# Kernel optimization log

Hardware: AMD Instinct MI355X
Metric: run time of the kernel (lower is better)

Reference implementation:

```python
import jax, jax.numpy as jnp
import numpy as np

B, N, E, H = 2, 2048, 2048, 16
D = E // H  # head_dim = 128


def setup_inputs() -> dict:
    key = jax.random.key(0)
    k1, k2, k3, k4 = jax.random.split(key, 4)
    x = jax.random.normal(k1, (B, N, E), dtype=jnp.float32)
    Wq = jax.random.normal(k2, (E, E), dtype=jnp.float32) * 0.02
    Wkv = jax.random.normal(k3, (2 * E, E), dtype=jnp.float32) * 0.02
    Wout = jax.random.normal(k4, (E, E), dtype=jnp.float32) * 0.02
    return {"x": x, "Wq": Wq, "Wkv": Wkv, "Wout": Wout}


def reference(x, Wq, Wkv, Wout):
    # projections (torch Linear: y = x @ W.T)
    q = x @ Wq.T                      # [b, n, e]
    kv = x @ Wkv.T                    # [b, n, 2e]
    k, v = jnp.split(kv, 2, axis=-1)  # each [b, n, e]

    def split_heads(t):
        return t.reshape(B, N, H, D).transpose(0, 2, 1, 3)  # [b, h, n, d]

    q, k, v = split_heads(q), split_heads(k), split_heads(v)

    scale = D ** -0.5
    sim = jnp.einsum('bhid,bhjd->bhij', q * scale, k)  # [b, h, n, n]

    # causal mask: triu(j - i + 1) masks strictly-future positions
    mask_value = -jnp.finfo(sim.dtype).max
    causal_mask = jnp.triu(jnp.ones((N, N), dtype=bool), k=1)
    sim = jnp.where(causal_mask, mask_value, sim)

    attn = jax.nn.softmax(sim, axis=-1)
    out = jnp.einsum('bhij,bhjd->bhid', attn, v)  # [b, h, n, d]
    out = out.transpose(0, 2, 1, 3).reshape(B, N, E)
    return out @ Wout.T
```

## Files before the change

kernel.cpp:

```cpp
#include <hip/hip_runtime.h>


typedef __bf16 bf16;
typedef bf16 bf16x4 __attribute__((ext_vector_type(4)));
typedef bf16 bf16x8 __attribute__((ext_vector_type(8)));
typedef float f32x4 __attribute__((ext_vector_type(4)));
typedef float f32x16 __attribute__((ext_vector_type(16)));

typedef const __attribute__((address_space(1))) void cg_void;
typedef __attribute__((address_space(3))) void lds_void;

#define MFMA16(a, b, c) __builtin_amdgcn_mfma_f32_16x16x32_bf16((a), (b), (c), 0, 0, 0)
#define MFMA32(a, b, c) __builtin_amdgcn_mfma_f32_32x32x16_bf16((a), (b), (c), 0, 0, 0)

__device__ __forceinline__ void async_load16(const bf16* g, bf16* l) {
  __builtin_amdgcn_global_load_lds((cg_void*)g, (lds_void*)l, 16, 0, 0);
}

__global__ __launch_bounds__(256) void cast_all_kernel(
    const float* __restrict__ x, const float* __restrict__ wq,
    const float* __restrict__ wkv, const float* __restrict__ wout,
    bf16* __restrict__ xb, bf16* __restrict__ wqkvb, bf16* __restrict__ woutb) {
  long i = (long)blockIdx.x * 256 + threadIdx.x;
  const float* src; bf16* dst; long off;
  if (i < 1048576)      { src = x;    dst = xb;            off = i; }
  else if (i < 2621440) { src = wq;   dst = wqkvb;         off = i - 1048576;
                          if (off >= 524288) { src = wkv; dst = wqkvb + 4194304; off -= 524288; } }
  else                  { src = wout; dst = woutb;         off = i - 2621440; }
  float4 f0 = ((const float4*)src)[2 * off];
  float4 f1 = ((const float4*)src)[2 * off + 1];
  bf16x8 o;
  o[0] = (bf16)f0.x; o[1] = (bf16)f0.y; o[2] = (bf16)f0.z; o[3] = (bf16)f0.w;
  o[4] = (bf16)f1.x; o[5] = (bf16)f1.y; o[6] = (bf16)f1.z; o[7] = (bf16)f1.w;
  ((bf16x8*)dst)[off] = o;
}

template <typename OutT>
__global__ __launch_bounds__(256, 2)
void gemm_bt_kernel(const bf16* __restrict__ A, const bf16* __restrict__ B,
                    OutT* __restrict__ C, int K, int NN) {
  __shared__ __attribute__((aligned(16))) bf16 As[128 * 32];
  __shared__ __attribute__((aligned(16))) bf16 Bs[128 * 32];
  const int tid = threadIdx.x;
  const int wave = tid >> 6, lane = tid & 63;
  const int quad = lane >> 4, l15 = lane & 15;
  const int m0 = blockIdx.y * 128, n0 = blockIdx.x * 128;
  const int wm = (wave >> 1) * 64, wn = (wave & 1) * 64;

  f32x4 acc[4][4];
#pragma unroll
  for (int i = 0; i < 4; ++i)
#pragma unroll
    for (int j = 0; j < 4; ++j) acc[i][j] = {0.f, 0.f, 0.f, 0.f};

  const int srow = tid >> 2;
  const int scol = (tid & 3) * 8;
  const bf16* aG = A + (size_t)(m0 + srow) * K + scol;
  const bf16* bG = B + (size_t)(n0 + srow) * K + scol;
  bf16* aL = As + srow * 32 + scol;
  bf16* bL = Bs + srow * 32 + scol;
  const size_t gstep = (size_t)64 * K;

  for (int kt = 0; kt < K; kt += 32) {
    __syncthreads();
    async_load16(aG, aL);
    async_load16(aG + gstep, aL + 64 * 32);
    async_load16(bG, bL);
    async_load16(bG + gstep, bL + 64 * 32);
    aG += 32; bG += 32;
    __syncthreads();

    bf16x8 af[4], bfr[4];
#pragma unroll
    for (int i = 0; i < 4; ++i)
      af[i] = *(const bf16x8*)(As + (wm + i * 16 + l15) * 32 + quad * 8);
#pragma unroll
    for (int j = 0; j < 4; ++j)
      bfr[j] = *(const bf16x8*)(Bs + (wn + j * 16 + l15) * 32 + quad * 8);
#pragma unroll
    for (int i = 0; i < 4; ++i)
#pragma unroll
      for (int j = 0; j < 4; ++j) acc[i][j] = MFMA16(af[i], bfr[j], acc[i][j]);
  }

#pragma unroll
  for (int i = 0; i < 4; ++i) {
#pragma unroll
    for (int r = 0; r < 4; ++r) {
      int row = m0 + wm + i * 16 + quad * 4 + r;
      size_t base = (size_t)row * NN + n0 + wn + l15;
#pragma unroll
      for (int j = 0; j < 4; ++j) C[base + j * 16] = (OutT)acc[i][j][r];
    }
  }
}

__global__ __launch_bounds__(256) void vtrans_kernel(const bf16* __restrict__ qkvb,
                                                     bf16* __restrict__ vt) {
  constexpr int QKV = 6144, NSEQ = 2048, E = 2048;
  __shared__ __attribute__((aligned(16))) bf16 Ts[64 * 64];
  const int t = threadIdx.x;
  const int n0 = blockIdx.x * 64, f0 = blockIdx.y * 64, bb = blockIdx.z;
#pragma unroll
  for (int p = 0; p < 2; ++p) {
    int c = p * 256 + t;
    int i = c >> 3, jc = c & 7;
    bf16x8 v = *(const bf16x8*)(qkvb + (size_t)(bb * NSEQ + n0 + i) * QKV + 4096 + f0 + jc * 8);
    *(bf16x8*)(Ts + i * 64 + ((jc + i) & 7) * 8) = v;
  }
  __syncthreads();
#pragma unroll
  for (int p = 0; p < 2; ++p) {
    int c = p * 256 + t;
    int fl = c >> 3, nl = (c & 7) * 8;
    bf16x8 o;
#pragma unroll
    for (int k = 0; k < 8; ++k) {
      int row = nl + k;
      o[k] = Ts[row * 64 + (((fl >> 3) + row) & 7) * 8 + (fl & 7)];
    }
    *(bf16x8*)(vt + (size_t)(bb * E + f0 + fl) * NSEQ + n0 + nl) = o;
  }
}

__global__ __launch_bounds__(128, 2)
void attn_kernel(const bf16* __restrict__ qkv, const bf16* __restrict__ vt,
                 bf16* __restrict__ yb) {
  constexpr int NSEQ = 2048, E = 2048, QKV = 6144;
  __shared__ __attribute__((aligned(16))) bf16 Ks[64 * 128];
  __shared__ __attribute__((aligned(16))) bf16 Vs[128 * 64];
  __shared__ __attribute__((aligned(16))) bf16 Ps[2][32 * 64];
  const int tid = threadIdx.x;
  const int wave = tid >> 6, lane = tid & 63;
  const int l31 = lane & 31, half = lane >> 5;
  const int b = blockIdx.x >> 4, h = blockIdx.x & 15;
  const int slot = blockIdx.y, qsub = slot & 7, g = slot >> 3;
  const int qt = (g == 0) ? qsub : (g == 1) ? 15 - qsub : (g == 2) ? 16 + qsub : 31 - qsub;
  const float c1 = 0.08838834764831845f * 1.44269504088896f;

  const int qrow = qt * 64 + wave * 32 + l31;
  bf16x8 qf[8];
  {
    const bf16* qp = qkv + (size_t)(b * NSEQ + qrow) * QKV + h * 128 + half * 8;
#pragma unroll
    for (int k8 = 0; k8 < 8; ++k8) qf[k8] = *(const bf16x8*)(qp + k8 * 16);
  }

  float m = -3.0e38f, l = 0.f;
  f32x16 accO[4];
#pragma unroll
  for (int md = 0; md < 4; ++md)
#pragma unroll
    for (int r = 0; r < 16; ++r) accO[md][r] = 0.f;

  bf16* psw = Ps[wave];
  const int ksr = tid >> 4, kss = tid & 15;
  const int vsr = tid >> 3, vss = tid & 7;
  bf16* kdst = Ks + tid * 8;
  bf16* vdst = Vs + tid * 8;

  for (int kt = 0; kt <= qt; ++kt) {
    __syncthreads();
#pragma unroll
    for (int p = 0; p < 8; ++p) {
      int r = p * 8 + ksr;
      int gch = kss ^ (r & 7);
      const bf16* gsrc = qkv + (size_t)(b * NSEQ + kt * 64 + r) * QKV + 2048 + h * 128 + gch * 8;
      async_load16(gsrc, kdst + p * 1024);
    }
#pragma unroll
    for (int p = 0; p < 8; ++p) {
      int r = p * 16 + vsr;
      int gch = vss ^ (r & 7);
      const bf16* gsrc = vt + ((size_t)b * E + h * 128 + r) * NSEQ + kt * 64 + gch * 8;
      async_load16(gsrc, vdst + p * 1024);
    }
    __syncthreads();

    f32x16 st[2];
#pragma unroll
    for (int mt = 0; mt < 2; ++mt)
#pragma unroll
      for (int r = 0; r < 16; ++r) st[mt][r] = 0.f;
#pragma unroll
    for (int k8 = 0; k8 < 8; ++k8) {
#pragma unroll
      for (int mt = 0; mt < 2; ++mt) {
        int row = mt * 32 + l31;
        int sl = (k8 * 2 + half) ^ (row & 7);
        bf16x8 kf = *(const bf16x8*)(Ks + row * 128 + sl * 8);
        st[mt] = MFMA32(kf, qf[k8], st[mt]);
      }
    }

    if (kt == qt) {
#pragma unroll
      for (int mt = 0; mt < 2; ++mt)
#pragma unroll
        for (int r = 0; r < 16; ++r) {
          int t = kt * 64 + mt * 32 + (r & 3) + 8 * (r >> 2) + 4 * half;
          if (t > qrow) st[mt][r] = -3.0e38f;
        }
    }

    float mx = -3.0e38f;
#pragma unroll
    for (int mt = 0; mt < 2; ++mt)
#pragma unroll
      for (int r = 0; r < 16; ++r) mx = fmaxf(mx, st[mt][r]);
    mx = fmaxf(mx, __shfl_xor(mx, 32));
    float mnew = fmaxf(m, mx);
    float alpha = exp2f((m - mnew) * c1);
    float mc = mnew * c1;
    m = mnew;
    float psum = 0.f;
#pragma unroll
    for (int mt = 0; mt < 2; ++mt)
#pragma unroll
      for (int r = 0; r < 16; ++r) {
        float p = exp2f(st[mt][r] * c1 - mc);
        psum += p;
        int t = mt * 32 + (r & 3) + 8 * (r >> 2) + 4 * half;
        psw[l31 * 64 + ((t >> 3) ^ (l31 & 7)) * 8 + (t & 7)] = (bf16)p;
      }
    psum += __shfl_xor(psum, 32);
    l = l * alpha + psum;

    if (alpha != 1.0f) {
#pragma unroll
      for (int md = 0; md < 4; ++md)
#pragma unroll
        for (int r = 0; r < 16; ++r) accO[md][r] *= alpha;
    }

    bf16x8 pf[4];
#pragma unroll
    for (int kk = 0; kk < 4; ++kk) {
      int sl = (kk * 2 + half) ^ (l31 & 7);
      pf[kk] = *(const bf16x8*)(psw + l31 * 64 + sl * 8);
    }
#pragma unroll
    for (int md = 0; md < 4; ++md) {
      int row = md * 32 + l31;
#pragma unroll
      for (int kk = 0; kk < 4; ++kk) {
        int sl = (kk * 2 + half) ^ (row & 7);
        bf16x8 vf = *(const bf16x8*)(Vs + row * 64 + sl * 8);
        accO[md] = MFMA32(vf, pf[kk], accO[md]);
      }
    }
  }

  float invl = 1.0f / l;
  bf16* yp = yb + (size_t)(b * NSEQ + qrow) * E + h * 128;
#pragma unroll
  for (int md = 0; md < 4; ++md)
#pragma unroll
    for (int rq = 0; rq < 4; ++rq) {
      bf16x4 o;
#pragma unroll
      for (int i = 0; i < 4; ++i) o[i] = (bf16)(accO[md][rq * 4 + i] * invl);
      *(bf16x4*)(yp + md * 32 + rq * 8 + half * 4) = o;
    }
}

extern "C" void kernel_launch(void* const* d_in, const int* in_sizes, int n_in,
                              void* d_out, int out_size, void* d_ws, size_t ws_size,
                              hipStream_t stream) {
  const float* x    = (const float*)d_in[0];
  const float* Wq   = (const float*)d_in[1];
  const float* Wkv  = (const float*)d_in[2];
  const float* Wout = (const float*)d_in[3];
  float* out = (float*)d_out;

  constexpr size_t NX = (size_t)2 * 2048 * 2048;
  constexpr size_t NW = (size_t)2048 * 2048;

  bf16* xb     = (bf16*)d_ws;
  bf16* wqkvb  = xb + NX;
  bf16* woutb  = wqkvb + 3 * NW;
  bf16* qkv_b  = woutb + NW;
  bf16* y_b    = qkv_b + 3 * NX;
  bf16* vt_b   = xb;

  cast_all_kernel<<<12288, 256, 0, stream>>>(x, Wq, Wkv, Wout, xb, wqkvb, woutb);

  gemm_bt_kernel<bf16><<<dim3(48, 32), 256, 0, stream>>>(xb, wqkvb, qkv_b, 2048, 6144);
  vtrans_kernel<<<dim3(32, 32, 2), 256, 0, stream>>>(qkv_b, vt_b);
  attn_kernel<<<dim3(32, 32), 128, 0, stream>>>(qkv_b, vt_b, y_b);
  gemm_bt_kernel<float><<<dim3(16, 32), 256, 0, stream>>>(y_b, woutb, out, 2048, 2048);
}
```

Before: 393.3 us.

## Widen attention tiles to 128 query rows and pass P through registers

The attention block now has 4 waves covering 128 query rows, so each K/V tile loaded into LDS is shared by twice as many queries. The P matrix no longer goes through LDS; it is rebuilt as the MFMA operand from registers using lane shuffles. The causal tile ordering is reworked for 16 slots, and GEMM launch bounds are raised to allow 4 blocks per CU. The risks are waves sitting idle on the diagonal tile, an unconditional alpha rescale, and more register pressure in the GEMM.

Result: faster. 384.0 us (-2.3%).

```diff
diff --git a/kernel.cpp b/kernel.cpp
--- a/kernel.cpp
+++ b/kernel.cpp
@@ -2,6 +2,7 @@
 
 
 typedef __bf16 bf16;
+typedef bf16 bf16x2 __attribute__((ext_vector_type(2)));
 typedef bf16 bf16x4 __attribute__((ext_vector_type(4)));
 typedef bf16 bf16x8 __attribute__((ext_vector_type(8)));
 typedef float f32x4 __attribute__((ext_vector_type(4)));
@@ -36,7 +37,7 @@
 }
 
 template <typename OutT>
-__global__ __launch_bounds__(256, 2)
+__global__ __launch_bounds__(256, 4)
 void gemm_bt_kernel(const bf16* __restrict__ A, const bf16* __restrict__ B,
                     OutT* __restrict__ C, int K, int NN) {
   __shared__ __attribute__((aligned(16))) bf16 As[128 * 32];
@@ -123,22 +124,21 @@
   }
 }
 
-__global__ __launch_bounds__(128, 2)
+__global__ __launch_bounds__(256, 2)
 void attn_kernel(const bf16* __restrict__ qkv, const bf16* __restrict__ vt,
                  bf16* __restrict__ yb) {
   constexpr int NSEQ = 2048, E = 2048, QKV = 6144;
   __shared__ __attribute__((aligned(16))) bf16 Ks[64 * 128];
   __shared__ __attribute__((aligned(16))) bf16 Vs[128 * 64];
-  __shared__ __attribute__((aligned(16))) bf16 Ps[2][32 * 64];
   const int tid = threadIdx.x;
   const int wave = tid >> 6, lane = tid & 63;
   const int l31 = lane & 31, half = lane >> 5;
   const int b = blockIdx.x >> 4, h = blockIdx.x & 15;
-  const int slot = blockIdx.y, qsub = slot & 7, g = slot >> 3;
-  const int qt = (g == 0) ? qsub : (g == 1) ? 15 - qsub : (g == 2) ? 16 + qsub : 31 - qsub;
+  const int slot = blockIdx.y;
+  const int qt = (slot < 8) ? slot : 23 - slot;
   const float c1 = 0.08838834764831845f * 1.44269504088896f;
 
-  const int qrow = qt * 64 + wave * 32 + l31;
+  const int qrow = qt * 128 + wave * 32 + l31;
   bf16x8 qf[8];
   {
     const bf16* qp = qkv + (size_t)(b * NSEQ + qrow) * QKV + h * 128 + half * 8;
@@ -153,29 +153,36 @@
 #pragma unroll
     for (int r = 0; r < 16; ++r) accO[md][r] = 0.f;
 
-  bf16* psw = Ps[wave];
-  const int ksr = tid >> 4, kss = tid & 15;
-  const int vsr = tid >> 3, vss = tid & 7;
+  const int krow_s = tid >> 4, kch_s = tid & 15;
+  const int vrow_s = tid >> 3, vch_s = tid & 7;
   bf16* kdst = Ks + tid * 8;
   bf16* vdst = Vs + tid * 8;
 
-  for (int kt = 0; kt <= qt; ++kt) {
+  const int diag = 2 * qt + (wave >> 1);
+  const int ktmax = 2 * qt + 1;
+
+  union PU { unsigned u; bf16x2 h; };
+  union FU { bf16x8 v; unsigned u[4]; };
+
+  for (int kt = 0; kt <= ktmax; ++kt) {
     __syncthreads();
 #pragma unroll
-    for (int p = 0; p < 8; ++p) {
-      int r = p * 8 + ksr;
-      int gch = kss ^ (r & 7);
+    for (int p = 0; p < 4; ++p) {
+      int r = p * 16 + krow_s;
+      int gch = kch_s ^ (r & 7);
       const bf16* gsrc = qkv + (size_t)(b * NSEQ + kt * 64 + r) * QKV + 2048 + h * 128 + gch * 8;
-      async_load16(gsrc, kdst + p * 1024);
-    }
-#pragma unroll
-    for (int p = 0; p < 8; ++p) {
-      int r = p * 16 + vsr;
-      int gch = vss ^ (r & 7);
+      async_load16(gsrc, kdst + p * 2048);
+    }
+#pragma unroll
+    for (int p = 0; p < 4; ++p) {
+      int r = p * 32 + vrow_s;
+      int gch = vch_s ^ (r & 7);
       const bf16* gsrc = vt + ((size_t)b * E + h * 128 + r) * NSEQ + kt * 64 + gch * 8;
-      async_load16(gsrc, vdst + p * 1024);
+      async_load16(gsrc, vdst + p * 2048);
     }
     __syncthreads();
+
+    if (kt > diag) continue;
 
     f32x16 st[2];
 #pragma unroll
@@ -193,7 +200,7 @@
       }
     }
 
-    if (kt == qt) {
+    if (kt == diag) {
 #pragma unroll
       for (int mt = 0; mt < 2; ++mt)
 #pragma unroll
@@ -213,42 +220,51 @@
     float alpha = exp2f((m - mnew) * c1);
     float mc = mnew * c1;
     m = mnew;
+
     float psum = 0.f;
+    unsigned pown[2][4][2];
 #pragma unroll
     for (int mt = 0; mt < 2; ++mt)
 #pragma unroll
-      for (int r = 0; r < 16; ++r) {
-        float p = exp2f(st[mt][r] * c1 - mc);
-        psum += p;
-        int t = mt * 32 + (r & 3) + 8 * (r >> 2) + 4 * half;
-        psw[l31 * 64 + ((t >> 3) ^ (l31 & 7)) * 8 + (t & 7)] = (bf16)p;
-      }
+      for (int qd = 0; qd < 4; ++qd)
+#pragma unroll
+        for (int pr = 0; pr < 2; ++pr) {
+          float p0 = exp2f(st[mt][qd * 4 + pr * 2] * c1 - mc);
+          float p1 = exp2f(st[mt][qd * 4 + pr * 2 + 1] * c1 - mc);
+          psum += p0 + p1;
+          PU a; a.h[0] = (bf16)p0; a.h[1] = (bf16)p1;
+          pown[mt][qd][pr] = a.u;
+        }
     psum += __shfl_xor(psum, 32);
     l = l * alpha + psum;
 
-    if (alpha != 1.0f) {
-#pragma unroll
-      for (int md = 0; md < 4; ++md)
-#pragma unroll
-        for (int r = 0; r < 16; ++r) accO[md][r] *= alpha;
-    }
-
-    bf16x8 pf[4];
-#pragma unroll
-    for (int kk = 0; kk < 4; ++kk) {
-      int sl = (kk * 2 + half) ^ (l31 & 7);
-      pf[kk] = *(const bf16x8*)(psw + l31 * 64 + sl * 8);
-    }
-#pragma unroll
-    for (int md = 0; md < 4; ++md) {
-      int row = md * 32 + l31;
-#pragma unroll
-      for (int kk = 0; kk < 4; ++kk) {
-        int sl = (kk * 2 + half) ^ (row & 7);
-        bf16x8 vf = *(const bf16x8*)(Vs + row * 64 + sl * 8);
-        accO[md] = MFMA32(vf, pf[kk], accO[md]);
+#pragma unroll
+    for (int md = 0; md < 4; ++md)
+#pragma unroll
+      for (int r = 0; r < 16; ++r) accO[md][r] *= alpha;
+
+#pragma unroll
+    for (int mt = 0; mt < 2; ++mt)
+#pragma unroll
+      for (int c = 0; c < 2; ++c) {
+        const int qa = 2 * c, qb = 2 * c + 1;
+        unsigned ra0 = __shfl_xor(pown[mt][qa][0], 32);
+        unsigned ra1 = __shfl_xor(pown[mt][qa][1], 32);
+        unsigned rb0 = __shfl_xor(pown[mt][qb][0], 32);
+        unsigned rb1 = __shfl_xor(pown[mt][qb][1], 32);
+        FU f;
+        f.u[0] = half ? rb0 : pown[mt][qa][0];
+        f.u[1] = half ? rb1 : pown[mt][qa][1];
+        f.u[2] = half ? pown[mt][qb][0] : ra0;
+        f.u[3] = half ? pown[mt][qb][1] : ra1;
+        const int kk = mt * 2 + c;
+#pragma unroll
+        for (int md = 0; md < 4; ++md) {
+          int row = md * 32 + l31;
+          bf16x8 vf = *(const bf16x8*)(Vs + row * 64 + (((kk * 2 + half) ^ (row & 7)) * 8));
+          accO[md] = MFMA32(vf, f.v, accO[md]);
+        }
       }
-    }
   }
 
   float invl = 1.0f / l;
@@ -287,6 +303,6 @@
 
   gemm_bt_kernel<bf16><<<dim3(48, 32), 256, 0, stream>>>(xb, wqkvb, qkv_b, 2048, 6144);
   vtrans_kernel<<<dim3(32, 32, 2), 256, 0, stream>>>(qkv_b, vt_b);
-  attn_kernel<<<dim3(32, 32), 128, 0, stream>>>(qkv_b, vt_b, y_b);
+  attn_kernel<<<dim3(32, 16), 256, 0, stream>>>(qkv_b, vt_b, y_b);
   gemm_bt_kernel<float><<<dim3(16, 32), 256, 0, stream>>>(y_b, woutb, out, 2048, 2048);
 }
```
